# Performance work log

Measured on AMD Instinct MI355X. Metric: run time of the kernel, lower is better.

The kernel has to match this reference:

```python
import jax, jax.numpy as jnp
import numpy as np

N_HEAD = 8
D_MODEL = 512
D_QKV = 64
LN_EPS = 1e-6


def setup_inputs() -> dict:
    key = jax.random.key(0)
    ks = jax.random.split(key, 10)
    B, S = 4, 2048
    q = jax.random.normal(ks[0], (B, S, D_MODEL), dtype=jnp.float32)
    k = jax.random.normal(ks[1], (B, S, D_MODEL), dtype=jnp.float32)
    v = jax.random.normal(ks[2], (B, S, D_MODEL), dtype=jnp.float32)
    mask = jax.random.randint(ks[3], (B, S, S), 0, 2, dtype=jnp.int32)
    scale = 1.0 / np.sqrt(D_MODEL)
    Wq = jax.random.normal(ks[4], (D_MODEL, N_HEAD * D_QKV), dtype=jnp.float32) * scale
    Wk = jax.random.normal(ks[5], (D_MODEL, N_HEAD * D_QKV), dtype=jnp.float32) * scale
    Wv = jax.random.normal(ks[6], (D_MODEL, N_HEAD * D_QKV), dtype=jnp.float32) * scale
    Wfc = jax.random.normal(ks[7], (N_HEAD * D_QKV, D_MODEL), dtype=jnp.float32) * scale
    gamma = jnp.ones((D_MODEL,), dtype=jnp.float32)
    beta = jnp.zeros((D_MODEL,), dtype=jnp.float32)
    return {"q": q, "k": k, "v": v, "mask": mask, "Wq": Wq, "Wk": Wk,
            "Wv": Wv, "Wfc": Wfc, "gamma": gamma, "beta": beta}


def _layer_norm(x, gamma, beta):
    mu = jnp.mean(x, axis=-1, keepdims=True)
    var = jnp.mean(jnp.square(x - mu), axis=-1, keepdims=True)
    return (x - mu) * jax.lax.rsqrt(var + LN_EPS) * gamma + beta


def reference(q, k, v, mask, Wq, Wk, Wv, Wfc, gamma, beta):
    B, Sq, _ = q.shape
    Sk = k.shape[1]
    residual = q
    qn = _layer_norm(q, gamma, beta)
    # projections -> [B, S, H, Dk]
    qh = (qn @ Wq).reshape(B, Sq, N_HEAD, D_QKV)
    kh = (k @ Wk).reshape(B, Sk, N_HEAD, D_QKV)
    vh = (v @ Wv).reshape(B, Sk, N_HEAD, D_QKV)
    temp = jnp.float32(D_QKV ** 0.5)
    # scores: [B, H, Sq, Sk]
    attn = jnp.einsum('bqhd,bkhd->bhqk', qh / temp, kh)
    attn = jnp.where(mask[:, None, :, :] == 0, jnp.float32(-1e9), attn)
    attn = jax.nn.softmax(attn, axis=-1)
    out = jnp.einsum('bhqk,bkhd->bqhd', attn, vh).reshape(B, Sq, N_HEAD * D_QKV)
    out = out @ Wfc
    return out + residual
```

## Files before the change

### kernel.cpp

```cpp
#include <hip/hip_runtime.h>

#define BATCH 4
#define SEQ   2048
#define NHEAD 8
#define DQKV  64
#define DMODEL 512
#define ROWS  (BATCH*SEQ)
#define BH    (BATCH*NHEAD)
#define HSTRIDE (SEQ*DQKV)

using f32x4  = __attribute__((ext_vector_type(4))) float;
using short8 = __attribute__((ext_vector_type(8))) short;
using short4v = __attribute__((ext_vector_type(4))) short;

#define MFMA16(a,b,c) __builtin_amdgcn_mfma_f32_16x16x32_bf16((a),(b),(c),0,0,0)

__device__ __forceinline__ short f2bf(float f) {
    unsigned u = __float_as_uint(f);
    u += 0x7FFFu + ((u >> 16) & 1u);
    return (short)(u >> 16);
}

__device__ __forceinline__ void gl2lds16(const short* g, short* l) {
    __builtin_amdgcn_global_load_lds(
        (__attribute__((address_space(1))) void*)g,
        (__attribute__((address_space(3))) void*)l, 16, 0, 0);
}

__device__ __forceinline__ void stage64x64(const short* g0, int gstride, short* lt, int t) {
    #pragma unroll
    for (int p = 0; p < 2; ++p) {
        int o = p * 2048 + t * 8;
        int row = o >> 6;
        int c = ((o >> 3) & 7) ^ (row & 7);
        gl2lds16(g0 + (size_t)row * gstride + c * 8, lt + o);
    }
}

__device__ __forceinline__ short8 trd(const short* t, int row, int c) {
    return *(const short8*)(t + row * 64 + ((c ^ (row & 7)) << 3));
}

__global__ __launch_bounds__(256) void prep_kernel(
        const float* __restrict__ q, const float* __restrict__ k,
        const float* __restrict__ v, const float* __restrict__ gamma,
        const float* __restrict__ beta,
        short* __restrict__ qn, short* __restrict__ kb, short* __restrict__ vb) {
    if (blockIdx.y == 0) {
        int wave = threadIdx.x >> 6, lane = threadIdx.x & 63;
        int row  = blockIdx.x * 4 + wave;
        const float4* qr = (const float4*)(q + (size_t)row * DMODEL);
        float4 x0 = qr[lane * 2];
        float4 x1 = qr[lane * 2 + 1];
        float s  = x0.x + x0.y + x0.z + x0.w + x1.x + x1.y + x1.z + x1.w;
        float s2 = x0.x*x0.x + x0.y*x0.y + x0.z*x0.z + x0.w*x0.w
                 + x1.x*x1.x + x1.y*x1.y + x1.z*x1.z + x1.w*x1.w;
        #pragma unroll
        for (int m = 1; m < 64; m <<= 1) {
            s  += __shfl_xor(s,  m);
            s2 += __shfl_xor(s2, m);
        }
        float mu  = s * (1.0f / DMODEL);
        float var = s2 * (1.0f / DMODEL) - mu * mu;
        float rstd = rsqrtf(var + 1e-6f);
        const float4* g = (const float4*)gamma;
        const float4* be = (const float4*)beta;
        float4 g0 = g[lane*2], g1 = g[lane*2+1];
        float4 b0 = be[lane*2], b1 = be[lane*2+1];
        short8 o;
        o[0] = f2bf((x0.x - mu) * rstd * g0.x + b0.x);
        o[1] = f2bf((x0.y - mu) * rstd * g0.y + b0.y);
        o[2] = f2bf((x0.z - mu) * rstd * g0.z + b0.z);
        o[3] = f2bf((x0.w - mu) * rstd * g0.w + b0.w);
        o[4] = f2bf((x1.x - mu) * rstd * g1.x + b1.x);
        o[5] = f2bf((x1.y - mu) * rstd * g1.y + b1.y);
        o[6] = f2bf((x1.z - mu) * rstd * g1.z + b1.z);
        o[7] = f2bf((x1.w - mu) * rstd * g1.w + b1.w);
        ((short8*)(qn + (size_t)row * DMODEL))[lane] = o;
    } else {
        const float* src = (blockIdx.y == 1) ? k : v;
        short* dst = (blockIdx.y == 1) ? kb : vb;
        size_t i = (size_t)blockIdx.x * 2048 + (size_t)threadIdx.x * 8;
        float4 a = *(const float4*)(src + i);
        float4 b = *(const float4*)(src + i + 4);
        short8 o;
        o[0]=f2bf(a.x); o[1]=f2bf(a.y); o[2]=f2bf(a.z); o[3]=f2bf(a.w);
        o[4]=f2bf(b.x); o[5]=f2bf(b.y); o[6]=f2bf(b.z); o[7]=f2bf(b.w);
        *(short8*)(dst + i) = o;
    }
}

__global__ __launch_bounds__(256) void castWT4_kernel(
        const float* __restrict__ W0, const float* __restrict__ W1,
        const float* __restrict__ W2, const float* __restrict__ W3,
        short* __restrict__ T0, short* __restrict__ T1,
        short* __restrict__ T2, short* __restrict__ T3) {
    __shared__ short tile[64 * 68];
    int w = blockIdx.z;
    const float* W = w==0 ? W0 : w==1 ? W1 : w==2 ? W2 : W3;
    short* T = w==0 ? T0 : w==1 ? T1 : w==2 ? T2 : T3;
    int ti = blockIdx.x, tj = blockIdx.y;
    int tid = threadIdx.x;
    #pragma unroll
    for (int p = 0; p < 4; ++p) {
        int idx = tid + p * 256;
        int kl = idx >> 4, c4 = idx & 15;
        float4 f = *(const float4*)(W + (size_t)(tj*64 + kl) * DMODEL + ti*64 + c4*4);
        short4v s; s[0]=f2bf(f.x); s[1]=f2bf(f.y); s[2]=f2bf(f.z); s[3]=f2bf(f.w);
        *(short4v*)(tile + kl*68 + c4*4) = s;
    }
    __syncthreads();
    #pragma unroll
    for (int p = 0; p < 4; ++p) {
        int idx = tid + p * 256;
        int nl = idx >> 4, kseg = idx & 15;
        short4v s;
        #pragma unroll
        for (int i = 0; i < 4; ++i) s[i] = tile[(kseg*4 + i)*68 + nl];
        *(short4v*)(T + (size_t)(ti*64 + nl) * DMODEL + tj*64 + kseg*4) = s;
    }
}

__global__ __launch_bounds__(256) void maskpack_kernel(
        const int* __restrict__ mask, unsigned long long* __restrict__ mp) {
    int gw = blockIdx.x * 4 + (threadIdx.x >> 6);
    int lane = threadIdx.x & 63;
    int r   = gw & 3;
    int rg  = (gw >> 2) & 1;
    int w64 = (gw >> 3) & 31;
    int qg  = (gw >> 8) & 63;
    int b   = gw >> 14;
    int row = qg * 32 + rg * 16 + (lane >> 4) * 4 + r;
    const int* src = mask + ((size_t)b * SEQ + row) * SEQ + w64 * 64 + (lane & 15);
    unsigned long long w0 = __ballot(src[0]  != 0);
    unsigned long long w1 = __ballot(src[16] != 0);
    unsigned long long w2 = __ballot(src[32] != 0);
    unsigned long long w3 = __ballot(src[48] != 0);
    if (lane == 0) {
        unsigned long long* d = mp + (size_t)gw * 4;
        d[0] = w0; d[1] = w1; d[2] = w2; d[3] = w3;
    }
}

__global__ __launch_bounds__(256, 4) void proj_qkv_kernel(
        const short* __restrict__ qn, const short* __restrict__ kb,
        const short* __restrict__ vb,
        const short* __restrict__ Wqt, const short* __restrict__ Wkt,
        const short* __restrict__ Wvt,
        short* __restrict__ qhp, short* __restrict__ khp, short* __restrict__ vtp) {
    __shared__ __align__(16) short Wl[2 * 4096];
    int tid = threadIdx.x, wave = tid >> 6, lane = tid & 63;
    int lm = lane & 15, lg = lane >> 4;
    int which = blockIdx.y >> 3;
    int CB0 = (blockIdx.y & 7) * 64;
    const short* A  = which==0 ? qn  : which==1 ? kb  : vb;
    const short* Wt = which==0 ? Wqt : which==1 ? Wkt : Wvt;
    float scale = which==0 ? 0.18033688f : 1.0f;

    int RBw = blockIdx.x * 128 + wave * 32;
    const short* Arow0 = A + (size_t)(RBw + lm) * DMODEL;
    const short* Arow1 = A + (size_t)(RBw + 16 + lm) * DMODEL;
    const short* W0 = Wt + (size_t)CB0 * DMODEL;

    short8 a[2][2];
    a[0][0] = *(const short8*)(Arow0 + lg * 8);
    a[0][1] = *(const short8*)(Arow0 + 32 + lg * 8);
    a[1][0] = *(const short8*)(Arow1 + lg * 8);
    a[1][1] = *(const short8*)(Arow1 + 32 + lg * 8);
    stage64x64(W0, DMODEL, Wl, tid);
    __syncthreads();

    f32x4 acc[2][4] = {};
    for (int kk = 0; kk < DMODEL; kk += 64) {
        int cur = (kk >> 6) & 1;
        bool more = (kk + 64) < DMODEL;
        short8 an[2][2];
        if (more) {
            stage64x64(W0 + kk + 64, DMODEL, Wl + (cur ^ 1) * 4096, tid);
            an[0][0] = *(const short8*)(Arow0 + kk + 64 + lg * 8);
            an[0][1] = *(const short8*)(Arow0 + kk + 96 + lg * 8);
            an[1][0] = *(const short8*)(Arow1 + kk + 64 + lg * 8);
            an[1][1] = *(const short8*)(Arow1 + kk + 96 + lg * 8);
        }
        const short* Wc = Wl + cur * 4096;
        #pragma unroll
        for (int cg = 0; cg < 4; ++cg) {
            short8 b0 = trd(Wc, cg*16 + lm, lg);
            short8 b1 = trd(Wc, cg*16 + lm, lg + 4);
            #pragma unroll
            for (int rg = 0; rg < 2; ++rg) {
                acc[rg][cg] = MFMA16(a[rg][0], b0, acc[rg][cg]);
                acc[rg][cg] = MFMA16(a[rg][1], b1, acc[rg][cg]);
            }
        }
        if (more) {
            #pragma unroll
            for (int rg = 0; rg < 2; ++rg) { a[rg][0] = an[rg][0]; a[rg][1] = an[rg][1]; }
        }
        __syncthreads();
    }

    if (which < 2) {
        short* outh = which==0 ? qhp : khp;
        #pragma unroll
        for (int rg = 0; rg < 2; ++rg) {
            #pragma unroll
            for (int cg = 0; cg < 4; ++cg) {
                int n = CB0 + cg * 16 + lm;
                int h = n >> 6, d = n & 63;
                #pragma unroll
                for (int r = 0; r < 4; ++r) {
                    int m = RBw + rg * 16 + lg * 4 + r;
                    int bb = m >> 11, s = m & 2047;
                    outh[(size_t)(bb * NHEAD + h) * HSTRIDE + (size_t)s * DQKV + d] =
                        f2bf(acc[rg][cg][r] * scale);
                }
            }
        }
    } else {
        int bb = RBw >> 11;
        #pragma unroll
        for (int rg = 0; rg < 2; ++rg) {
            int s0 = (RBw + rg * 16 + lg * 4) & 2047;
            #pragma unroll
            for (int cg = 0; cg < 4; ++cg) {
                int n = CB0 + cg * 16 + lm;
                int h = n >> 6, d = n & 63;
                short4v pk;
                #pragma unroll
                for (int r = 0; r < 4; ++r) pk[r] = f2bf(acc[rg][cg][r]);
                *(short4v*)(vtp + (size_t)(bb * NHEAD + h) * HSTRIDE
                            + (size_t)d * SEQ + s0) = pk;
            }
        }
    }
}

__global__ __launch_bounds__(256, 2) void attn_kernel(
        const short* __restrict__ qh, const short* __restrict__ kh,
        const short* __restrict__ vt, const unsigned long long* __restrict__ mpack,
        short* __restrict__ oh) {
    __shared__ __align__(16) short lds[24576];
    int tid = threadIdx.x, wave = tid >> 6, lane = tid & 63;
    int lm = lane & 15, lg = lane >> 4;
    int qt = blockIdx.x, bh = blockIdx.y, b = bh >> 3;
    int qbase = qt * 128 + wave * 32;
    short* Pw = lds + 16384 + wave * 2048;

    const short* Kbase = kh + (size_t)bh * HSTRIDE;
    const short* Vtb   = vt + (size_t)bh * HSTRIDE;

    short8 aq[2][2];
    #pragma unroll
    for (int rg = 0; rg < 2; ++rg) {
        const short8* Qrow = (const short8*)(qh + (size_t)bh * HSTRIDE
                              + (size_t)(qbase + rg * 16 + lm) * DQKV);
        aq[rg][0] = Qrow[lg];
        aq[rg][1] = Qrow[lg + 4];
    }

    int qg = __builtin_amdgcn_readfirstlane(qt * 4 + wave);
    const unsigned long long* mbase = mpack + (size_t)(b * 64 + qg) * 1024;

    const short one = (short)0x3F80;
    short8 ones = {one, one, one, one, one, one, one, one};

    f32x4 o[2][4] = {};
    f32x4 ox[2] = {};

    stage64x64(Kbase, DQKV, lds, tid);
    stage64x64(Vtb,   SEQ,  lds + 8192, tid);
    __syncthreads();

    for (int kt = 0; kt < SEQ; kt += 64) {
        int cur = (kt >> 6) & 1;
        if (kt + 64 < SEQ) {
            int nxt = cur ^ 1;
            stage64x64(Kbase + (size_t)(kt + 64) * DQKV, DQKV, lds + nxt * 4096, tid);
            stage64x64(Vtb + kt + 64, SEQ, lds + 8192 + nxt * 4096, tid);
        }
        const short* Kc = lds + cur * 4096;
        const short* Vc = lds + 8192 + cur * 4096;

        f32x4 sk[2][4];
        #pragma unroll
        for (int kg = 0; kg < 4; ++kg) {
            short8 bk0 = trd(Kc, kg*16 + lm, lg);
            short8 bk1 = trd(Kc, kg*16 + lm, lg + 4);
            #pragma unroll
            for (int rg = 0; rg < 2; ++rg) {
                f32x4 z{};
                z = MFMA16(aq[rg][0], bk0, z);
                sk[rg][kg] = MFMA16(aq[rg][1], bk1, z);
            }
        }

        const unsigned long long* mw = mbase + (kt >> 6) * 32;
        #pragma unroll
        for (int rg = 0; rg < 2; ++rg) {
            #pragma unroll
            for (int r = 0; r < 4; ++r) {
                int row = rg * 16 + lg * 4 + r;
                short* pd = Pw + row * 64 + (lm & 7);
                #pragma unroll
                for (int kg = 0; kg < 4; ++kg) {
                    unsigned long long mword = mw[rg * 16 + r * 4 + kg];
                    float e = __builtin_amdgcn_exp2f(sk[rg][kg][r]);
                    float pe;
                    asm("v_cndmask_b32 %0, 0, %1, %2" : "=v"(pe) : "v"(e), "s"(mword));
                    int c = (2 * kg + (lm >> 3)) ^ (row & 7);
                    pd[c * 8] = (short)(__float_as_uint(pe) >> 16);
                }
            }
        }

        short8 ap[2][2];
        #pragma unroll
        for (int rg = 0; rg < 2; ++rg) {
            ap[rg][0] = trd(Pw, rg*16 + lm, lg);
            ap[rg][1] = trd(Pw, rg*16 + lm, lg + 4);
        }

        #pragma unroll
        for (int dt = 0; dt < 4; ++dt) {
            short8 bv0 = trd(Vc, dt*16 + lm, lg);
            short8 bv1 = trd(Vc, dt*16 + lm, lg + 4);
            #pragma unroll
            for (int rg = 0; rg < 2; ++rg) {
                o[rg][dt] = MFMA16(ap[rg][0], bv0, o[rg][dt]);
                o[rg][dt] = MFMA16(ap[rg][1], bv1, o[rg][dt]);
            }
        }
        #pragma unroll
        for (int rg = 0; rg < 2; ++rg) {
            ox[rg] = MFMA16(ap[rg][0], ones, ox[rg]);
            ox[rg] = MFMA16(ap[rg][1], ones, ox[rg]);
        }
        __syncthreads();
    }

    short* ob = oh + (size_t)bh * HSTRIDE;
    #pragma unroll
    for (int rg = 0; rg < 2; ++rg) {
        float rinv[4];
        #pragma unroll
        for (int r = 0; r < 4; ++r) rinv[r] = __builtin_amdgcn_rcpf(ox[rg][r]);
        #pragma unroll
        for (int dt = 0; dt < 4; ++dt) {
            #pragma unroll
            for (int r = 0; r < 4; ++r) {
                ob[(size_t)(qbase + rg * 16 + lg * 4 + r) * DQKV + dt * 16 + lm] =
                    f2bf(o[rg][dt][r] * rinv[r]);
            }
        }
    }
}

__global__ __launch_bounds__(256, 4) void outproj_kernel(
        const short* __restrict__ Ah, const short* __restrict__ Wfct,
        const float* __restrict__ resid, float* __restrict__ out) {
    __shared__ __align__(16) short Wl[2 * 4096];
    int tid = threadIdx.x, wave = tid >> 6, lane = tid & 63;
    int lm = lane & 15, lg = lane >> 4;
    int CB0 = blockIdx.y * 64;
    int RBw = blockIdx.x * 128 + wave * 32;
    const short* W0 = Wfct + (size_t)CB0 * DMODEL;

    size_t rb[2];
    #pragma unroll
    for (int rg = 0; rg < 2; ++rg) {
        int m = RBw + rg * 16 + lm;
        rb[rg] = (size_t)(m >> 11) * (NHEAD * HSTRIDE) + (size_t)(m & 2047) * DQKV;
    }

    short8 a[2][2];
    #pragma unroll
    for (int rg = 0; rg < 2; ++rg) {
        a[rg][0] = *(const short8*)(Ah + rb[rg] + lg * 8);
        a[rg][1] = *(const short8*)(Ah + rb[rg] + 32 + lg * 8);
    }
    stage64x64(W0, DMODEL, Wl, tid);
    __syncthreads();

    f32x4 acc[2][4] = {};
    for (int kk = 0; kk < DMODEL; kk += 64) {
        int cur = (kk >> 6) & 1;
        bool more = (kk + 64) < DMODEL;
        short8 an[2][2];
        if (more) {
            stage64x64(W0 + kk + 64, DMODEL, Wl + (cur ^ 1) * 4096, tid);
            size_t hoff = (size_t)((kk >> 6) + 1) * HSTRIDE;
            #pragma unroll
            for (int rg = 0; rg < 2; ++rg) {
                an[rg][0] = *(const short8*)(Ah + rb[rg] + hoff + lg * 8);
                an[rg][1] = *(const short8*)(Ah + rb[rg] + hoff + 32 + lg * 8);
            }
        }
        const short* Wc = Wl + cur * 4096;
        #pragma unroll
        for (int cg = 0; cg < 4; ++cg) {
            short8 b0 = trd(Wc, cg*16 + lm, lg);
            short8 b1 = trd(Wc, cg*16 + lm, lg + 4);
            #pragma unroll
            for (int rg = 0; rg < 2; ++rg) {
                acc[rg][cg] = MFMA16(a[rg][0], b0, acc[rg][cg]);
                acc[rg][cg] = MFMA16(a[rg][1], b1, acc[rg][cg]);
            }
        }
        if (more) {
            #pragma unroll
            for (int rg = 0; rg < 2; ++rg) { a[rg][0] = an[rg][0]; a[rg][1] = an[rg][1]; }
        }
        __syncthreads();
    }

    #pragma unroll
    for (int rg = 0; rg < 2; ++rg) {
        #pragma unroll
        for (int cg = 0; cg < 4; ++cg) {
            int n = CB0 + cg * 16 + lm;
            #pragma unroll
            for (int r = 0; r < 4; ++r) {
                int m = RBw + rg * 16 + lg * 4 + r;
                size_t idx = (size_t)m * DMODEL + n;
                out[idx] = acc[rg][cg][r] + resid[idx];
            }
        }
    }
}

extern "C" void kernel_launch(void* const* d_in, const int* in_sizes, int n_in,
                              void* d_out, int out_size, void* d_ws, size_t ws_size,
                              hipStream_t stream) {
    const float* q     = (const float*)d_in[0];
    const float* k     = (const float*)d_in[1];
    const float* v     = (const float*)d_in[2];
    const int*   mask  = (const int*)d_in[3];
    const float* Wq    = (const float*)d_in[4];
    const float* Wk    = (const float*)d_in[5];
    const float* Wv    = (const float*)d_in[6];
    const float* Wfc   = (const float*)d_in[7];
    const float* gamma = (const float*)d_in[8];
    const float* beta  = (const float*)d_in[9];
    float* out = (float*)d_out;

    char* ws = (char*)d_ws;
    const size_t SZ_ROWS = (size_t)ROWS * DMODEL * sizeof(short);
    const size_t SZ_W    = (size_t)DMODEL * DMODEL * sizeof(short);
    short* qn   = (short*)(ws);
    short* kbf  = (short*)(ws + SZ_ROWS);
    short* vbf  = (short*)(ws + 2 * SZ_ROWS);
    short* Wqt  = (short*)(ws + 3 * SZ_ROWS);
    short* Wkt  = (short*)(ws + 3 * SZ_ROWS + SZ_W);
    short* Wvt  = (short*)(ws + 3 * SZ_ROWS + 2 * SZ_W);
    short* Wfct = (short*)(ws + 3 * SZ_ROWS + 3 * SZ_W);
    short* qhb  = (short*)(ws + 3 * SZ_ROWS + 4 * SZ_W);
    short* khb  = (short*)(ws + 4 * SZ_ROWS + 4 * SZ_W);
    short* vtb  = (short*)(ws + 5 * SZ_ROWS + 4 * SZ_W);
    unsigned long long* mpack = (unsigned long long*)(ws + 6 * SZ_ROWS + 4 * SZ_W);
    short* aout = qn;

    prep_kernel<<<dim3(ROWS / 4, 3), 256, 0, stream>>>(q, k, v, gamma, beta, qn, kbf, vbf);
    castWT4_kernel<<<dim3(8, 8, 4), 256, 0, stream>>>(Wq, Wk, Wv, Wfc, Wqt, Wkt, Wvt, Wfct);
    maskpack_kernel<<<65536 / 4, 256, 0, stream>>>(mask, mpack);

    proj_qkv_kernel<<<dim3(ROWS / 128, 24), 256, 0, stream>>>(
        qn, kbf, vbf, Wqt, Wkt, Wvt, qhb, khb, vtb);

    attn_kernel<<<dim3(SEQ / 128, BH), 256, 0, stream>>>(qhb, khb, vtb, mpack, aout);

    outproj_kernel<<<dim3(ROWS / 128, DMODEL / 64), 256, 0, stream>>>(aout, Wfct, q, out);
}
```

Measured before the change: 284.1 us.

## Retile QKV projection, attention, and output projection for different reuse/occupancy balance

```diff
diff --git a/kernel.cpp b/kernel.cpp
--- a/kernel.cpp
+++ b/kernel.cpp
@@ -35,6 +35,10 @@
         int c = ((o >> 3) & 7) ^ (row & 7);
         gl2lds16(g0 + (size_t)row * gstride + c * 8, lt + o);
     }
+}
+__device__ __forceinline__ void stage128x64(const short* g0, int gstride, short* lt, int t) {
+    stage64x64(g0, gstride, lt, t);
+    stage64x64(g0 + (size_t)64 * gstride, gstride, lt + 4096, t);
 }
 
 __device__ __forceinline__ short8 trd(const short* t, int row, int c) {
@@ -148,11 +152,11 @@
         const short* __restrict__ Wqt, const short* __restrict__ Wkt,
         const short* __restrict__ Wvt,
         short* __restrict__ qhp, short* __restrict__ khp, short* __restrict__ vtp) {
-    __shared__ __align__(16) short Wl[2 * 4096];
+    __shared__ __align__(16) short Wl[2 * 8192];
     int tid = threadIdx.x, wave = tid >> 6, lane = tid & 63;
     int lm = lane & 15, lg = lane >> 4;
-    int which = blockIdx.y >> 3;
-    int CB0 = (blockIdx.y & 7) * 64;
+    int which = blockIdx.y >> 2;
+    int CB0 = (blockIdx.y & 3) * 128;
     const short* A  = which==0 ? qn  : which==1 ? kb  : vb;
     const short* Wt = which==0 ? Wqt : which==1 ? Wkt : Wvt;
     float scale = which==0 ? 0.18033688f : 1.0f;
@@ -167,24 +171,24 @@
     a[0][1] = *(const short8*)(Arow0 + 32 + lg * 8);
     a[1][0] = *(const short8*)(Arow1 + lg * 8);
     a[1][1] = *(const short8*)(Arow1 + 32 + lg * 8);
-    stage64x64(W0, DMODEL, Wl, tid);
+    stage128x64(W0, DMODEL, Wl, tid);
     __syncthreads();
 
-    f32x4 acc[2][4] = {};
+    f32x4 acc[2][8] = {};
     for (int kk = 0; kk < DMODEL; kk += 64) {
         int cur = (kk >> 6) & 1;
         bool more = (kk + 64) < DMODEL;
         short8 an[2][2];
         if (more) {
-            stage64x64(W0 + kk + 64, DMODEL, Wl + (cur ^ 1) * 4096, tid);
+            stage128x64(W0 + kk + 64, DMODEL, Wl + (cur ^ 1) * 8192, tid);
             an[0][0] = *(const short8*)(Arow0 + kk + 64 + lg * 8);
             an[0][1] = *(const short8*)(Arow0 + kk + 96 + lg * 8);
             an[1][0] = *(const short8*)(Arow1 + kk + 64 + lg * 8);
             an[1][1] = *(const short8*)(Arow1 + kk + 96 + lg * 8);
         }
-        const short* Wc = Wl + cur * 4096;
-        #pragma unroll
-        for (int cg = 0; cg < 4; ++cg) {
+        const short* Wc = Wl + cur * 8192;
+        #pragma unroll
+        for (int cg = 0; cg < 8; ++cg) {
             short8 b0 = trd(Wc, cg*16 + lm, lg);
             short8 b1 = trd(Wc, cg*16 + lm, lg + 4);
             #pragma unroll
@@ -205,7 +209,7 @@
         #pragma unroll
         for (int rg = 0; rg < 2; ++rg) {
             #pragma unroll
-            for (int cg = 0; cg < 4; ++cg) {
+            for (int cg = 0; cg < 8; ++cg) {
                 int n = CB0 + cg * 16 + lm;
                 int h = n >> 6, d = n & 63;
                 #pragma unroll
@@ -223,7 +227,7 @@
         for (int rg = 0; rg < 2; ++rg) {
             int s0 = (RBw + rg * 16 + lg * 4) & 2047;
             #pragma unroll
-            for (int cg = 0; cg < 4; ++cg) {
+            for (int cg = 0; cg < 8; ++cg) {
                 int n = CB0 + cg * 16 + lm;
                 int h = n >> 6, d = n & 63;
                 short4v pk;
@@ -236,37 +240,34 @@
     }
 }
 
-__global__ __launch_bounds__(256, 2) void attn_kernel(
+__global__ __launch_bounds__(256, 4) void attn_kernel(
         const short* __restrict__ qh, const short* __restrict__ kh,
         const short* __restrict__ vt, const unsigned long long* __restrict__ mpack,
         short* __restrict__ oh) {
-    __shared__ __align__(16) short lds[24576];
+    __shared__ __align__(16) short lds[20480];
     int tid = threadIdx.x, wave = tid >> 6, lane = tid & 63;
     int lm = lane & 15, lg = lane >> 4;
     int qt = blockIdx.x, bh = blockIdx.y, b = bh >> 3;
-    int qbase = qt * 128 + wave * 32;
-    short* Pw = lds + 16384 + wave * 2048;
+    int qbase = qt * 64 + wave * 16;
+    short* Pw = lds + 16384 + wave * 1024;
 
     const short* Kbase = kh + (size_t)bh * HSTRIDE;
     const short* Vtb   = vt + (size_t)bh * HSTRIDE;
 
-    short8 aq[2][2];
-    #pragma unroll
-    for (int rg = 0; rg < 2; ++rg) {
-        const short8* Qrow = (const short8*)(qh + (size_t)bh * HSTRIDE
-                              + (size_t)(qbase + rg * 16 + lm) * DQKV);
-        aq[rg][0] = Qrow[lg];
-        aq[rg][1] = Qrow[lg + 4];
-    }
-
-    int qg = __builtin_amdgcn_readfirstlane(qt * 4 + wave);
-    const unsigned long long* mbase = mpack + (size_t)(b * 64 + qg) * 1024;
+    const short8* Qrow = (const short8*)(qh + (size_t)bh * HSTRIDE
+                          + (size_t)(qbase + lm) * DQKV);
+    short8 aq0 = Qrow[lg];
+    short8 aq1 = Qrow[lg + 4];
+
+    int mblk = __builtin_amdgcn_readfirstlane(
+        ((b * 64 + qt * 2 + (wave >> 1)) << 10) + ((wave & 1) << 4));
+    const unsigned long long* mbase = mpack + mblk;
 
     const short one = (short)0x3F80;
     short8 ones = {one, one, one, one, one, one, one, one};
 
-    f32x4 o[2][4] = {};
-    f32x4 ox[2] = {};
+    f32x4 o[4] = {};
+    f32x4 ox{};
 
     stage64x64(Kbase, DQKV, lds, tid);
     stage64x64(Vtb,   SEQ,  lds + 8192, tid);
@@ -282,76 +283,57 @@
         const short* Kc = lds + cur * 4096;
         const short* Vc = lds + 8192 + cur * 4096;
 
-        f32x4 sk[2][4];
+        f32x4 sk[4];
         #pragma unroll
         for (int kg = 0; kg < 4; ++kg) {
             short8 bk0 = trd(Kc, kg*16 + lm, lg);
             short8 bk1 = trd(Kc, kg*16 + lm, lg + 4);
+            f32x4 z{};
+            z = MFMA16(aq0, bk0, z);
+            sk[kg] = MFMA16(aq1, bk1, z);
+        }
+
+        const unsigned long long* mw = mbase + (kt >> 6) * 32;
+        #pragma unroll
+        for (int r = 0; r < 4; ++r) {
+            int row = lg * 4 + r;
+            short* pd = Pw + row * 64 + (lm & 7);
             #pragma unroll
-            for (int rg = 0; rg < 2; ++rg) {
-                f32x4 z{};
-                z = MFMA16(aq[rg][0], bk0, z);
-                sk[rg][kg] = MFMA16(aq[rg][1], bk1, z);
+            for (int kg = 0; kg < 4; ++kg) {
+                unsigned long long mword = mw[r * 4 + kg];
+                float e = __builtin_amdgcn_exp2f(sk[kg][r]);
+                float pe;
+                asm("v_cndmask_b32 %0, 0, %1, %2" : "=v"(pe) : "v"(e), "s"(mword));
+                int c = (2 * kg + (lm >> 3)) ^ (row & 7);
+                pd[c * 8] = f2bf(pe);
             }
         }
 
-        const unsigned long long* mw = mbase + (kt >> 6) * 32;
-        #pragma unroll
-        for (int rg = 0; rg < 2; ++rg) {
-            #pragma unroll
-            for (int r = 0; r < 4; ++r) {
-                int row = rg * 16 + lg * 4 + r;
-                short* pd = Pw + row * 64 + (lm & 7);
-                #pragma unroll
-                for (int kg = 0; kg < 4; ++kg) {
-                    unsigned long long mword = mw[rg * 16 + r * 4 + kg];
-                    float e = __builtin_amdgcn_exp2f(sk[rg][kg][r]);
-                    float pe;
-                    asm("v_cndmask_b32 %0, 0, %1, %2" : "=v"(pe) : "v"(e), "s"(mword));
-                    int c = (2 * kg + (lm >> 3)) ^ (row & 7);
-                    pd[c * 8] = (short)(__float_as_uint(pe) >> 16);
-                }
-            }
-        }
-
-        short8 ap[2][2];
-        #pragma unroll
-        for (int rg = 0; rg < 2; ++rg) {
-            ap[rg][0] = trd(Pw, rg*16 + lm, lg);
-            ap[rg][1] = trd(Pw, rg*16 + lm, lg + 4);
-        }
+        short8 ap0 = trd(Pw, lm, lg);
+        short8 ap1 = trd(Pw, lm, lg + 4);
 
         #pragma unroll
         for (int dt = 0; dt < 4; ++dt) {
             short8 bv0 = trd(Vc, dt*16 + lm, lg);
             short8 bv1 = trd(Vc, dt*16 + lm, lg + 4);
-            #pragma unroll
-            for (int rg = 0; rg < 2; ++rg) {
-                o[rg][dt] = MFMA16(ap[rg][0], bv0, o[rg][dt]);
-                o[rg][dt] = MFMA16(ap[rg][1], bv1, o[rg][dt]);
-            }
-        }
-        #pragma unroll
-        for (int rg = 0; rg < 2; ++rg) {
-            ox[rg] = MFMA16(ap[rg][0], ones, ox[rg]);
-            ox[rg] = MFMA16(ap[rg][1], ones, ox[rg]);
-        }
+            o[dt] = MFMA16(ap0, bv0, o[dt]);
+            o[dt] = MFMA16(ap1, bv1, o[dt]);
+        }
+        ox = MFMA16(ap0, ones, ox);
+        ox = MFMA16(ap1, ones, ox);
         __syncthreads();
     }
 
     short* ob = oh + (size_t)bh * HSTRIDE;
-    #pragma unroll
-    for (int rg = 0; rg < 2; ++rg) {
-        float rinv[4];
-        #pragma unroll
-        for (int r = 0; r < 4; ++r) rinv[r] = __builtin_amdgcn_rcpf(ox[rg][r]);
-        #pragma unroll
-        for (int dt = 0; dt < 4; ++dt) {
-            #pragma unroll
-            for (int r = 0; r < 4; ++r) {
-                ob[(size_t)(qbase + rg * 16 + lg * 4 + r) * DQKV + dt * 16 + lm] =
-                    f2bf(o[rg][dt][r] * rinv[r]);
-            }
+    float rinv[4];
+    #pragma unroll
+    for (int r = 0; r < 4; ++r) rinv[r] = __builtin_amdgcn_rcpf(ox[r]);
+    #pragma unroll
+    for (int dt = 0; dt < 4; ++dt) {
+        #pragma unroll
+        for (int r = 0; r < 4; ++r) {
+            ob[(size_t)(qbase + lg * 4 + r) * DQKV + dt * 16 + lm] =
+                f2bf(o[dt][r] * rinv[r]);
         }
     }
 }
@@ -363,68 +345,48 @@
     int tid = threadIdx.x, wave = tid >> 6, lane = tid & 63;
     int lm = lane & 15, lg = lane >> 4;
     int CB0 = blockIdx.y * 64;
-    int RBw = blockIdx.x * 128 + wave * 32;
+    int RB = blockIdx.x * 64 + wave * 16;
     const short* W0 = Wfct + (size_t)CB0 * DMODEL;
 
-    size_t rb[2];
-    #pragma unroll
-    for (int rg = 0; rg < 2; ++rg) {
-        int m = RBw + rg * 16 + lm;
-        rb[rg] = (size_t)(m >> 11) * (NHEAD * HSTRIDE) + (size_t)(m & 2047) * DQKV;
-    }
-
-    short8 a[2][2];
-    #pragma unroll
-    for (int rg = 0; rg < 2; ++rg) {
-        a[rg][0] = *(const short8*)(Ah + rb[rg] + lg * 8);
-        a[rg][1] = *(const short8*)(Ah + rb[rg] + 32 + lg * 8);
-    }
+    int m0 = RB + lm;
+    size_t rb = (size_t)(m0 >> 11) * (NHEAD * HSTRIDE) + (size_t)(m0 & 2047) * DQKV;
+
+    short8 a0 = *(const short8*)(Ah + rb + lg * 8);
+    short8 a1 = *(const short8*)(Ah + rb + 32 + lg * 8);
     stage64x64(W0, DMODEL, Wl, tid);
     __syncthreads();
 
-    f32x4 acc[2][4] = {};
+    f32x4 acc[4] = {};
     for (int kk = 0; kk < DMODEL; kk += 64) {
         int cur = (kk >> 6) & 1;
         bool more = (kk + 64) < DMODEL;
-        short8 an[2][2];
+        short8 a0n, a1n;
         if (more) {
             stage64x64(W0 + kk + 64, DMODEL, Wl + (cur ^ 1) * 4096, tid);
             size_t hoff = (size_t)((kk >> 6) + 1) * HSTRIDE;
-            #pragma unroll
-            for (int rg = 0; rg < 2; ++rg) {
-                an[rg][0] = *(const short8*)(Ah + rb[rg] + hoff + lg * 8);
-                an[rg][1] = *(const short8*)(Ah + rb[rg] + hoff + 32 + lg * 8);
-            }
+            a0n = *(const short8*)(Ah + rb + hoff + lg * 8);
+            a1n = *(const short8*)(Ah + rb + hoff + 32 + lg * 8);
         }
         const short* Wc = Wl + cur * 4096;
         #pragma unroll
         for (int cg = 0; cg < 4; ++cg) {
             short8 b0 = trd(Wc, cg*16 + lm, lg);
             short8 b1 = trd(Wc, cg*16 + lm, lg + 4);
-            #pragma unroll
-            for (int rg = 0; rg < 2; ++rg) {
-                acc[rg][cg] = MFMA16(a[rg][0], b0, acc[rg][cg]);
-                acc[rg][cg] = MFMA16(a[rg][1], b1, acc[rg][cg]);
-            }
-        }
-        if (more) {
-            #pragma unroll
-            for (int rg = 0; rg < 2; ++rg) { a[rg][0] = an[rg][0]; a[rg][1] = an[rg][1]; }
-        }
+            acc[cg] = MFMA16(a0, b0, acc[cg]);
+            acc[cg] = MFMA16(a1, b1, acc[cg]);
+        }
+        if (more) { a0 = a0n; a1 = a1n; }
         __syncthreads();
     }
 
     #pragma unroll
-    for (int rg = 0; rg < 2; ++rg) {
-        #pragma unroll
-        for (int cg = 0; cg < 4; ++cg) {
-            int n = CB0 + cg * 16 + lm;
-            #pragma unroll
-            for (int r = 0; r < 4; ++r) {
-                int m = RBw + rg * 16 + lg * 4 + r;
-                size_t idx = (size_t)m * DMODEL + n;
-                out[idx] = acc[rg][cg][r] + resid[idx];
-            }
+    for (int cg = 0; cg < 4; ++cg) {
+        int n = CB0 + cg * 16 + lm;
+        #pragma unroll
+        for (int r = 0; r < 4; ++r) {
+            int m = RB + lg * 4 + r;
+            size_t idx = (size_t)m * DMODEL + n;
+            out[idx] = acc[cg][r] + resid[idx];
         }
     }
 }
@@ -464,10 +426,10 @@
     castWT4_kernel<<<dim3(8, 8, 4), 256, 0, stream>>>(Wq, Wk, Wv, Wfc, Wqt, Wkt, Wvt, Wfct);
     maskpack_kernel<<<65536 / 4, 256, 0, stream>>>(mask, mpack);
 
-    proj_qkv_kernel<<<dim3(ROWS / 128, 24), 256, 0, stream>>>(
+    proj_qkv_kernel<<<dim3(ROWS / 128, 12), 256, 0, stream>>>(
         qn, kbf, vbf, Wqt, Wkt, Wvt, qhb, khb, vtb);
 
-    attn_kernel<<<dim3(SEQ / 128, BH), 256, 0, stream>>>(qhb, khb, vtb, mpack, aout);
-
-    outproj_kernel<<<dim3(ROWS / 128, DMODEL / 64), 256, 0, stream>>>(aout, Wfct, q, out);
-}
+    attn_kernel<<<dim3(SEQ / 64, BH), 256, 0, stream>>>(qhb, khb, vtb, mpack, aout);
+
+    outproj_kernel<<<dim3(ROWS / 64, DMODEL / 64), 256, 0, stream>>>(aout, Wfct, q, out);
+}
```

Result: faster. 261.9 us (-7.8%).
